# Kernel optimization log

Hardware: AMD Instinct MI355X
Metric: run time of the kernel (lower is better)

The kernel has to match this reference:

```python
import jax, jax.numpy as jnp
import numpy as np

# Layer node counts: [n0, n1, n2, n3] for a 3-hop sampled subgraph
N_NODES = [524288, 65536, 8192, 1024]
DIMS = [100, 256, 256, 47]


def sage_conv(x_src, x_dst, src, dst, Wl, bl, Wr, n_dst):
    # PyG SAGEConv: lin_l(mean_agg(neighbors)) + lin_r(root)
    msg = x_src[src]                                        # [E, in]
    agg = jax.ops.segment_sum(msg, dst, num_segments=n_dst)  # [n_dst, in]
    cnt = jax.ops.segment_sum(jnp.ones((src.shape[0],), dtype=x_src.dtype), dst,
                              num_segments=n_dst)
    agg = agg / jnp.maximum(cnt, 1.0)[:, None]               # mean, 0-deg -> 0
    return agg @ Wl + bl + x_dst @ Wr


def setup_inputs() -> dict:
    key = jax.random.key(0)
    ks = jax.random.split(key, 20)
    inp = {"x": jax.random.normal(ks[0], (N_NODES[0], DIMS[0]), dtype=jnp.float32)}
    E = [655360, 81920, 10240]
    for i in range(3):
        inp[f"src{i}"] = jax.random.randint(ks[1 + 2 * i], (E[i],), 0, N_NODES[i])
        inp[f"dst{i}"] = jax.random.randint(ks[2 + 2 * i], (E[i],), 0, N_NODES[i + 1])
    for i in range(3):
        fin, fout = DIMS[i], DIMS[i + 1]
        inp[f"Wl{i}"] = jax.random.normal(ks[7 + 3 * i], (fin, fout), jnp.float32) * (1.0 / np.sqrt(fin))
        inp[f"bl{i}"] = jnp.zeros((fout,), jnp.float32)
        inp[f"Wr{i}"] = jax.random.normal(ks[8 + 3 * i], (fin, fout), jnp.float32) * (1.0 / np.sqrt(fin))
    return inp


def reference(x, src0, dst0, src1, dst1, src2, dst2,
              Wl0, bl0, Wr0, Wl1, bl1, Wr1, Wl2, bl2, Wr2):
    srcs = [src0, src1, src2]
    dsts = [dst0, dst1, dst2]
    Wls = [Wl0, Wl1, Wl2]
    bls = [bl0, bl1, bl2]
    Wrs = [Wr0, Wr1, Wr2]
    h = x
    for i in range(3):
        n_dst = N_NODES[i + 1]
        h_dst = h[:n_dst]
        h = sage_conv(h, h_dst, srcs[i], dsts[i], Wls[i], bls[i], Wrs[i], n_dst)
        if i != 2:
            h = jax.nn.relu(h)  # dropout is identity in eval mode
    return jax.nn.log_softmax(h, axis=-1)
```

## Files before the change

kernel.cpp:

```cpp
#include <hip/hip_runtime.h>
#include <math.h>

constexpr int NN1 = 65536, NN2 = 8192, NN3 = 1024;
constexpr int E0 = 655360, E1 = 81920, E2 = 10240;
constexpr int ETOT = E0 + E1 + E2;
constexpr int NTOT = NN1 + NN2 + NN3;

static inline int cdiv(int a, int b) { return (a + b - 1) / b; }

typedef __bf16 bf16x8_t __attribute__((ext_vector_type(8)));
typedef float f32x4_t __attribute__((ext_vector_type(4)));

__device__ __forceinline__ unsigned short f2bf(float f) {
    union { float f; unsigned int u; } v; v.f = f;
    unsigned int r = v.u + 0x7fffu + ((v.u >> 16) & 1u);
    return (unsigned short)(r >> 16);
}
__device__ __forceinline__ float bf2f(unsigned short h) {
    union { unsigned int u; float f; } v; v.u = ((unsigned int)h) << 16;
    return v.f;
}

__global__ void count_all(const int* __restrict__ dst0, const int* __restrict__ dst1,
                          const int* __restrict__ dst2, int* __restrict__ cnt) {
    int i = blockIdx.x * 256 + threadIdx.x;
    if (i < E0) atomicAdd(&cnt[dst0[i]], 1);
    else if (i < E0 + E1) atomicAdd(&cnt[NN1 + dst1[i - E0]], 1);
    else if (i < ETOT) atomicAdd(&cnt[NN1 + NN2 + dst2[i - E0 - E1]], 1);
}

__global__ __launch_bounds__(1024) void scan1(const int* __restrict__ cnt, int n,
                                              int* __restrict__ ofs, int* __restrict__ sums) {
    __shared__ int s[1024];
    int i = blockIdx.x * 1024 + threadIdx.x;
    int v = (i < n) ? cnt[i] : 0;
    s[threadIdx.x] = v;
    __syncthreads();
    for (int off = 1; off < 1024; off <<= 1) {
        int t = (threadIdx.x >= off) ? s[threadIdx.x - off] : 0;
        __syncthreads();
        s[threadIdx.x] += t;
        __syncthreads();
    }
    if (i < n) ofs[i] = s[threadIdx.x] - v;
    if (threadIdx.x == 1023) sums[blockIdx.x] = s[1023];
}

__global__ void scan3(const int* __restrict__ sums, int n,
                      int* __restrict__ ofs, int* __restrict__ cursor) {
    __shared__ int pref_s;
    int c = (blockIdx.x * 256) >> 10;
    if (threadIdx.x < 64) {
        int v = 0;
        for (int j = threadIdx.x; j < c; j += 64) v += sums[j];
        for (int o = 32; o; o >>= 1) v += __shfl_down(v, o);
        if (threadIdx.x == 0) pref_s = v;
    }
    __syncthreads();
    int i = blockIdx.x * 256 + threadIdx.x;
    if (i < n) {
        int v = ofs[i] + pref_s;
        ofs[i] = v;
        cursor[i] = v;
    }
    if (blockIdx.x == 0 && threadIdx.x == 0) ofs[n] = ETOT;
}

__global__ void scatter_all(const int* __restrict__ src0, const int* __restrict__ dst0,
                            const int* __restrict__ src1, const int* __restrict__ dst1,
                            const int* __restrict__ src2, const int* __restrict__ dst2,
                            int* __restrict__ cursor, int* __restrict__ perm) {
    int i = blockIdx.x * 256 + threadIdx.x;
    if (i < E0) {
        int p = atomicAdd(&cursor[dst0[i]], 1);
        perm[p] = src0[i];
    } else if (i < E0 + E1) {
        int j = i - E0;
        int p = atomicAdd(&cursor[NN1 + dst1[j]], 1);
        perm[p] = src1[j];
    } else if (i < ETOT) {
        int j = i - E0 - E1;
        int p = atomicAdd(&cursor[NN1 + NN2 + dst2[j]], 1);
        perm[p] = src2[j];
    }
}

__global__ void agg0_kernel(const float* __restrict__ x, const int* __restrict__ perm,
                            const int* __restrict__ ofs, unsigned short* __restrict__ Ab, int nrows) {
    int wave = (blockIdx.x * blockDim.x + threadIdx.x) >> 6;
    int lane = threadIdx.x & 63;
    if (wave >= nrows) return;
    int g = lane >> 5, l5 = lane & 31;
    bool act = l5 < 25;
    int s0 = ofs[wave], s1 = ofs[wave + 1];
    float inv = 1.0f / fmaxf((float)(s1 - s0), 1.0f);
    f32x4_t A0 = {0.f, 0.f, 0.f, 0.f}, A1 = A0, A2 = A0, A3 = A0;
    int e = s0;
    for (; e + 8 <= s1; e += 8) {
        int p0 = perm[e + 0 + g];
        int p1 = perm[e + 2 + g];
        int p2 = perm[e + 4 + g];
        int p3 = perm[e + 6 + g];
        if (act) {
            A0 += *reinterpret_cast<const f32x4_t*>(x + (size_t)p0 * 100 + l5 * 4);
            A1 += *reinterpret_cast<const f32x4_t*>(x + (size_t)p1 * 100 + l5 * 4);
            A2 += *reinterpret_cast<const f32x4_t*>(x + (size_t)p2 * 100 + l5 * 4);
            A3 += *reinterpret_cast<const f32x4_t*>(x + (size_t)p3 * 100 + l5 * 4);
        }
    }
    for (; e < s1; e += 2) {
        int idx = e + g;
        if (idx < s1 && act)
            A0 += *reinterpret_cast<const f32x4_t*>(x + (size_t)perm[idx] * 100 + l5 * 4);
    }
    f32x4_t a = (A0 + A1) + (A2 + A3);
#pragma unroll
    for (int c = 0; c < 4; c++) a[c] += __shfl_xor(a[c], 32);
    unsigned short* row = Ab + (size_t)wave * 224;
    if (lane < 25) {
        ushort4 o;
        o.x = f2bf(a[0] * inv); o.y = f2bf(a[1] * inv);
        o.z = f2bf(a[2] * inv); o.w = f2bf(a[3] * inv);
        *reinterpret_cast<ushort4*>(row + lane * 4) = o;
        f32x4_t d = *reinterpret_cast<const f32x4_t*>(x + (size_t)wave * 100 + lane * 4);
        ushort4 od;
        od.x = f2bf(d[0]); od.y = f2bf(d[1]); od.z = f2bf(d[2]); od.w = f2bf(d[3]);
        *reinterpret_cast<ushort4*>(row + 100 + lane * 4) = od;
    } else if (lane < 31) {
        *reinterpret_cast<ushort4*>(row + 100 + lane * 4) = make_ushort4(0, 0, 0, 0);
    }
}

__global__ void agg1_kernel(const unsigned short* __restrict__ h, const int* __restrict__ perm,
                            const int* __restrict__ ofs, unsigned short* __restrict__ Ab, int nrows) {
    int wave = (blockIdx.x * blockDim.x + threadIdx.x) >> 6;
    int lane = threadIdx.x & 63;
    if (wave >= nrows) return;
    int s0 = ofs[wave], s1 = ofs[wave + 1];
    float inv = 1.0f / fmaxf((float)(s1 - s0), 1.0f);
    float acc[4][4] = {};
    int e = s0;
    for (; e + 4 <= s1; e += 4) {
        ushort4 v[4];
#pragma unroll
        for (int u = 0; u < 4; u++)
            v[u] = *reinterpret_cast<const ushort4*>(h + (size_t)perm[e + u] * 256 + lane * 4);
#pragma unroll
        for (int u = 0; u < 4; u++) {
            acc[u][0] += bf2f(v[u].x); acc[u][1] += bf2f(v[u].y);
            acc[u][2] += bf2f(v[u].z); acc[u][3] += bf2f(v[u].w);
        }
    }
    for (; e < s1; e++) {
        ushort4 v = *reinterpret_cast<const ushort4*>(h + (size_t)perm[e] * 256 + lane * 4);
        acc[0][0] += bf2f(v.x); acc[0][1] += bf2f(v.y);
        acc[0][2] += bf2f(v.z); acc[0][3] += bf2f(v.w);
    }
    ushort4 o;
    o.x = f2bf((acc[0][0] + acc[1][0] + acc[2][0] + acc[3][0]) * inv);
    o.y = f2bf((acc[0][1] + acc[1][1] + acc[2][1] + acc[3][1]) * inv);
    o.z = f2bf((acc[0][2] + acc[1][2] + acc[2][2] + acc[3][2]) * inv);
    o.w = f2bf((acc[0][3] + acc[1][3] + acc[2][3] + acc[3][3]) * inv);
    *reinterpret_cast<ushort4*>(Ab + (size_t)wave * 512 + lane * 4) = o;
    *reinterpret_cast<ushort4*>(Ab + (size_t)wave * 512 + 256 + lane * 4) =
        *reinterpret_cast<const ushort4*>(h + (size_t)wave * 256 + lane * 4);
}

__global__ void agg_vec4_256(const float* __restrict__ x, const int* __restrict__ perm,
                             const int* __restrict__ ofs, float* __restrict__ agg, int nrows) {
    int wave = (blockIdx.x * blockDim.x + threadIdx.x) >> 6;
    int lane = threadIdx.x & 63;
    if (wave >= nrows) return;
    int s0 = ofs[wave], s1 = ofs[wave + 1];
    float4 acc = make_float4(0.f, 0.f, 0.f, 0.f);
    for (int e = s0; e < s1; e++) {
        const float4* xr = (const float4*)(x + (size_t)perm[e] * 256);
        float4 v = xr[lane];
        acc.x += v.x; acc.y += v.y; acc.z += v.z; acc.w += v.w;
    }
    float inv = 1.0f / fmaxf((float)(s1 - s0), 1.0f);
    acc.x *= inv; acc.y *= inv; acc.z *= inv; acc.w *= inv;
    ((float4*)(agg + (size_t)wave * 256))[lane] = acc;
}

__global__ void prep_w(const float* __restrict__ Wl0, const float* __restrict__ Wr0,
                       unsigned short* __restrict__ Wt0,
                       const float* __restrict__ Wl1, const float* __restrict__ Wr1,
                       unsigned short* __restrict__ Wt1) {
    int b = blockIdx.x;
    if (b < 256) {
        int n = b, k = threadIdx.x;
        if (k < 224) {
            float v = (k < 100) ? Wl0[k * 256 + n] : (k < 200 ? Wr0[(k - 100) * 256 + n] : 0.f);
            Wt0[n * 224 + k] = f2bf(v);
        }
    } else {
        int idx = (b - 256) * 256 + threadIdx.x;
        int n = idx >> 9, k = idx & 511;
        float v = (k < 256) ? Wl1[k * 256 + n] : Wr1[(k - 256) * 256 + n];
        Wt1[idx] = f2bf(v);
    }
}

template <int OUT_BF16, int RELU>
__global__ __launch_bounds__(256) void mfma_gemm(const unsigned short* __restrict__ A,
                                                 const unsigned short* __restrict__ Wt,
                                                 const float* __restrict__ bias,
                                                 void* __restrict__ outp,
                                                 int M, int N, int K) {
    __shared__ unsigned short As[128][40];
    __shared__ unsigned short Bs[128][40];
    int tid = threadIdx.x;
    int lane = tid & 63, wid = tid >> 6;
    int wm = (wid & 1) * 64, wn = (wid >> 1) * 64;
    int bm = blockIdx.y * 128, bn = blockIdx.x * 128;

    f32x4_t acc[4][4];
#pragma unroll
    for (int i = 0; i < 4; i++)
#pragma unroll
        for (int j = 0; j < 4; j++)
#pragma unroll
            for (int r = 0; r < 4; r++) acc[i][j][r] = 0.f;

    int r0 = lane & 15, kg = lane >> 4;

    for (int k0 = 0; k0 < K; k0 += 32) {
        {
            int c = tid;
            int row = c >> 2, k8 = (c & 3) << 3;
            *reinterpret_cast<int4*>(&As[row][k8]) =
                *reinterpret_cast<const int4*>(&A[(size_t)(bm + row) * K + k0 + k8]);
            c = tid + 256;
            row = c >> 2; k8 = (c & 3) << 3;
            *reinterpret_cast<int4*>(&As[row][k8]) =
                *reinterpret_cast<const int4*>(&A[(size_t)(bm + row) * K + k0 + k8]);
        }
        {
            int c = tid;
            int row = c >> 2, k8 = (c & 3) << 3;
            *reinterpret_cast<int4*>(&Bs[row][k8]) =
                *reinterpret_cast<const int4*>(&Wt[(size_t)(bn + row) * K + k0 + k8]);
            c = tid + 256;
            row = c >> 2; k8 = (c & 3) << 3;
            *reinterpret_cast<int4*>(&Bs[row][k8]) =
                *reinterpret_cast<const int4*>(&Wt[(size_t)(bn + row) * K + k0 + k8]);
        }
        __syncthreads();

        bf16x8_t af[4], bfv[4];
#pragma unroll
        for (int mi = 0; mi < 4; mi++)
            af[mi] = *reinterpret_cast<const bf16x8_t*>(&As[wm + mi * 16 + r0][kg * 8]);
#pragma unroll
        for (int ni = 0; ni < 4; ni++)
            bfv[ni] = *reinterpret_cast<const bf16x8_t*>(&Bs[wn + ni * 16 + r0][kg * 8]);
#pragma unroll
        for (int mi = 0; mi < 4; mi++)
#pragma unroll
            for (int ni = 0; ni < 4; ni++)
                acc[mi][ni] = __builtin_amdgcn_mfma_f32_16x16x32_bf16(af[mi], bfv[ni], acc[mi][ni], 0, 0, 0);
        __syncthreads();
    }

    int cc = lane & 15, rr = (lane >> 4) * 4;
#pragma unroll
    for (int mi = 0; mi < 4; mi++) {
#pragma unroll
        for (int ni = 0; ni < 4; ni++) {
            int col = bn + wn + ni * 16 + cc;
            float b = bias[col];
#pragma unroll
            for (int j = 0; j < 4; j++) {
                int row = bm + wm + mi * 16 + rr + j;
                float v = acc[mi][ni][j] + b;
                if (RELU) v = fmaxf(v, 0.f);
                if (OUT_BF16)
                    ((unsigned short*)outp)[(size_t)row * N + col] = f2bf(v);
                else
                    ((float*)outp)[(size_t)row * N + col] = v;
            }
        }
    }
}

__global__ __launch_bounds__(256) void gemm2_fused(const float* __restrict__ A1, const float* __restrict__ W1, int K1,
                                                   const float* __restrict__ A2, const float* __restrict__ W2, int K2,
                                                   const float* __restrict__ bias, float* __restrict__ out,
                                                   int M, int N) {
    __shared__ float As[16][65];
    __shared__ float Bs[16][64];
    int tid = threadIdx.x;
    int tx = tid & 15, ty = tid >> 4;
    int bm = blockIdx.y * 64;
    float acc[4][4] = {};
    for (int pass = 0; pass < 2; ++pass) {
        const float* A = pass ? A2 : A1;
        const float* W = pass ? W2 : W1;
        int K = pass ? K2 : K1;
        for (int k0 = 0; k0 < K; k0 += 16) {
#pragma unroll
            for (int i = 0; i < 4; i++) {
                int L = i * 256 + tid;
                int m = L >> 4, k = L & 15;
                int gm = bm + m, gk = k0 + k;
                float v = 0.f;
                if (gm < M && gk < K) v = A[(size_t)gm * K + gk];
                As[k][m] = v;
            }
#pragma unroll
            for (int i = 0; i < 4; i++) {
                int L = i * 256 + tid;
                int n = L & 63, k = L >> 6;
                int gk = k0 + k;
                float v = 0.f;
                if (gk < K && n < N) v = W[(size_t)gk * N + n];
                Bs[k][n] = v;
            }
            __syncthreads();
#pragma unroll
            for (int k = 0; k < 16; k++) {
                float a[4], b[4];
#pragma unroll
                for (int i = 0; i < 4; i++) a[i] = As[k][ty * 4 + i];
#pragma unroll
                for (int j = 0; j < 4; j++) b[j] = Bs[k][tx * 4 + j];
#pragma unroll
                for (int i = 0; i < 4; i++)
#pragma unroll
                    for (int j = 0; j < 4; j++) acc[i][j] += a[i] * b[j];
            }
            __syncthreads();
        }
    }
#pragma unroll
    for (int i = 0; i < 4; i++) {
        int gm = bm + ty * 4 + i;
        float vals[4];
        float vmax = -1e30f;
#pragma unroll
        for (int j = 0; j < 4; j++) {
            int gn = tx * 4 + j;
            vals[j] = (gn < N) ? acc[i][j] + bias[gn] : -1e30f;
            vmax = fmaxf(vmax, vals[j]);
        }
#pragma unroll
        for (int o = 1; o < 16; o <<= 1) vmax = fmaxf(vmax, __shfl_xor(vmax, o));
        float se = 0.f;
#pragma unroll
        for (int j = 0; j < 4; j++) {
            int gn = tx * 4 + j;
            if (gn < N) se += expf(vals[j] - vmax);
        }
#pragma unroll
        for (int o = 1; o < 16; o <<= 1) se += __shfl_xor(se, o);
        float ls = logf(se);
#pragma unroll
        for (int j = 0; j < 4; j++) {
            int gn = tx * 4 + j;
            if (gn < N && gm < M) out[(size_t)gm * N + gn] = vals[j] - vmax - ls;
        }
    }
}

extern "C" void kernel_launch(void* const* d_in, const int* in_sizes, int n_in,
                              void* d_out, int out_size, void* d_ws, size_t ws_size,
                              hipStream_t stream) {
    const float* x   = (const float*)d_in[0];
    const int* src0  = (const int*)d_in[1];
    const int* dst0  = (const int*)d_in[2];
    const int* src1  = (const int*)d_in[3];
    const int* dst1  = (const int*)d_in[4];
    const int* src2  = (const int*)d_in[5];
    const int* dst2  = (const int*)d_in[6];
    const float* Wl0 = (const float*)d_in[7];
    const float* bl0 = (const float*)d_in[8];
    const float* Wr0 = (const float*)d_in[9];
    const float* Wl1 = (const float*)d_in[10];
    const float* bl1 = (const float*)d_in[11];
    const float* Wr1 = (const float*)d_in[12];
    const float* Wl2 = (const float*)d_in[13];
    const float* bl2 = (const float*)d_in[14];
    const float* Wr2 = (const float*)d_in[15];
    float* out = (float*)d_out;

    char* p = (char*)d_ws;
    auto alloc = [&](size_t bytes) { char* r = p; p += (bytes + 255) & ~(size_t)255; return r; };
    unsigned short* Ab0 = (unsigned short*)alloc((size_t)NN1 * 224 * 2);
    unsigned short* h1  = (unsigned short*)alloc((size_t)NN1 * 256 * 2);
    unsigned short* Ab1 = (unsigned short*)alloc((size_t)NN2 * 512 * 2);
    float* h2    = (float*)alloc((size_t)NN2 * 256 * 4);
    float* agg2  = (float*)alloc((size_t)NN3 * 256 * 4);
    unsigned short* Wt0 = (unsigned short*)alloc(256 * 224 * 2);
    unsigned short* Wt1 = (unsigned short*)alloc(256 * 512 * 2);
    int* cnt    = (int*)alloc((size_t)NTOT * 4);
    int* ofs    = (int*)alloc((size_t)(NTOT + 1) * 4);
    int* cursor = (int*)alloc((size_t)(NTOT + 1) * 4);
    int* sums   = (int*)alloc(128 * 4);
    int* perm   = (int*)alloc((size_t)ETOT * 4);

    prep_w<<<768, 256, 0, stream>>>(Wl0, Wr0, Wt0, Wl1, Wr1, Wt1);
    hipMemsetAsync(cnt, 0, (size_t)NTOT * 4, stream);
    count_all<<<cdiv(ETOT, 256), 256, 0, stream>>>(dst0, dst1, dst2, cnt);
    int nb = cdiv(NTOT, 1024);
    scan1<<<nb, 1024, 0, stream>>>(cnt, NTOT, ofs, sums);
    scan3<<<cdiv(NTOT, 256), 256, 0, stream>>>(sums, NTOT, ofs, cursor);
    scatter_all<<<cdiv(ETOT, 256), 256, 0, stream>>>(src0, dst0, src1, dst1, src2, dst2, cursor, perm);

    agg0_kernel<<<cdiv(NN1 * 64, 256), 256, 0, stream>>>(x, perm, ofs, Ab0, NN1);
    {
        dim3 grid(256 / 128, NN1 / 128);
        mfma_gemm<1, 1><<<grid, 256, 0, stream>>>(Ab0, Wt0, bl0, h1, NN1, 256, 224);
    }

    agg1_kernel<<<cdiv(NN2 * 64, 256), 256, 0, stream>>>(h1, perm, ofs + NN1, Ab1, NN2);
    {
        dim3 grid(256 / 128, NN2 / 128);
        mfma_gemm<0, 1><<<grid, 256, 0, stream>>>(Ab1, Wt1, bl1, h2, NN2, 256, 512);
    }

    agg_vec4_256<<<cdiv(NN3 * 64, 256), 256, 0, stream>>>(h2, perm, ofs + NN1 + NN2, agg2, NN3);
    {
        dim3 grid(1, cdiv(NN3, 64));
        gemm2_fused<<<grid, 256, 0, stream>>>(agg2, Wl2, 256, h2, Wr2, 256, bl2, out, NN3, 47);
    }
}
```

Before: 298.8 us.

## Fuse neighbor aggregation with MFMA GEMM for layers 0 and 1

Replaces the separate aggregate-then-GEMM kernels for layers 0 and 1 with fused kernels. Each block aggregates its own rows into shared memory and immediately runs the bf16 MFMA GEMM in two passes, first over the mean-aggregated features and then over the root features, so the concatenated A buffers are never written to or read back from global memory. Weights are split into separate left and right transposed bf16 matrices to match. The trade-off is that the gather and GEMM phases now run serially within a block with fewer blocks and larger shared memory, which may lower occupancy and latency hiding. In layer 1 the aggregation is also repeated by both column blocks.

```diff
diff --git a/kernel.cpp b/kernel.cpp
--- a/kernel.cpp
+++ b/kernel.cpp
@@ -85,85 +85,251 @@
     }
 }
 
-__global__ void agg0_kernel(const float* __restrict__ x, const int* __restrict__ perm,
-                            const int* __restrict__ ofs, unsigned short* __restrict__ Ab, int nrows) {
-    int wave = (blockIdx.x * blockDim.x + threadIdx.x) >> 6;
-    int lane = threadIdx.x & 63;
-    if (wave >= nrows) return;
-    int g = lane >> 5, l5 = lane & 31;
-    bool act = l5 < 25;
-    int s0 = ofs[wave], s1 = ofs[wave + 1];
-    float inv = 1.0f / fmaxf((float)(s1 - s0), 1.0f);
-    f32x4_t A0 = {0.f, 0.f, 0.f, 0.f}, A1 = A0, A2 = A0, A3 = A0;
-    int e = s0;
-    for (; e + 8 <= s1; e += 8) {
-        int p0 = perm[e + 0 + g];
-        int p1 = perm[e + 2 + g];
-        int p2 = perm[e + 4 + g];
-        int p3 = perm[e + 6 + g];
-        if (act) {
-            A0 += *reinterpret_cast<const f32x4_t*>(x + (size_t)p0 * 100 + l5 * 4);
-            A1 += *reinterpret_cast<const f32x4_t*>(x + (size_t)p1 * 100 + l5 * 4);
-            A2 += *reinterpret_cast<const f32x4_t*>(x + (size_t)p2 * 100 + l5 * 4);
-            A3 += *reinterpret_cast<const f32x4_t*>(x + (size_t)p3 * 100 + l5 * 4);
-        }
-    }
-    for (; e < s1; e += 2) {
-        int idx = e + g;
-        if (idx < s1 && act)
-            A0 += *reinterpret_cast<const f32x4_t*>(x + (size_t)perm[idx] * 100 + l5 * 4);
-    }
-    f32x4_t a = (A0 + A1) + (A2 + A3);
-#pragma unroll
-    for (int c = 0; c < 4; c++) a[c] += __shfl_xor(a[c], 32);
-    unsigned short* row = Ab + (size_t)wave * 224;
-    if (lane < 25) {
+__global__ void prep_w(const float* __restrict__ Wl0, const float* __restrict__ Wr0,
+                       unsigned short* __restrict__ Wt0a, unsigned short* __restrict__ Wt0b,
+                       const float* __restrict__ Wl1, const float* __restrict__ Wr1,
+                       unsigned short* __restrict__ Wt1a, unsigned short* __restrict__ Wt1b) {
+    int b = blockIdx.x, t = threadIdx.x;
+    if (b < 128) {
+        int idx = b * 256 + t; int n = idx >> 7, k = idx & 127;
+        Wt0a[idx] = f2bf(k < 100 ? Wl0[k * 256 + n] : 0.f);
+    } else if (b < 256) {
+        int idx = (b - 128) * 256 + t; int n = idx >> 7, k = idx & 127;
+        Wt0b[idx] = f2bf(k < 100 ? Wr0[k * 256 + n] : 0.f);
+    } else if (b < 512) {
+        int idx = (b - 256) * 256 + t; int n = idx >> 8, k = idx & 255;
+        Wt1a[idx] = f2bf(Wl1[k * 256 + n]);
+    } else {
+        int idx = (b - 512) * 256 + t; int n = idx >> 8, k = idx & 255;
+        Wt1b[idx] = f2bf(Wr1[k * 256 + n]);
+    }
+}
+
+__global__ __launch_bounds__(512) void fused_l0(const float* __restrict__ x,
+                                                const int* __restrict__ perm,
+                                                const int* __restrict__ ofs,
+                                                const unsigned short* __restrict__ Wt0a,
+                                                const unsigned short* __restrict__ Wt0b,
+                                                const float* __restrict__ bias,
+                                                unsigned short* __restrict__ h1) {
+    __shared__ unsigned short As[128][136];
+    __shared__ unsigned short Bs[256][40];
+    int tid = threadIdx.x;
+    int lane = tid & 63, wid = tid >> 6;
+    int bm = blockIdx.x * 128;
+
+    {
+        int g = lane >> 5, l5 = lane & 31;
+        bool act = l5 < 25;
+        for (int r = 0; r < 16; ++r) {
+            int row = wid * 16 + r;
+            int node = bm + row;
+            int s0 = ofs[node], s1 = ofs[node + 1];
+            float inv = 1.0f / fmaxf((float)(s1 - s0), 1.0f);
+            f32x4_t A0 = {0.f, 0.f, 0.f, 0.f}, A1 = A0, A2 = A0, A3 = A0;
+            int e = s0;
+            for (; e + 8 <= s1; e += 8) {
+                int p0 = perm[e + 0 + g];
+                int p1 = perm[e + 2 + g];
+                int p2 = perm[e + 4 + g];
+                int p3 = perm[e + 6 + g];
+                if (act) {
+                    A0 += *reinterpret_cast<const f32x4_t*>(x + (size_t)p0 * 100 + l5 * 4);
+                    A1 += *reinterpret_cast<const f32x4_t*>(x + (size_t)p1 * 100 + l5 * 4);
+                    A2 += *reinterpret_cast<const f32x4_t*>(x + (size_t)p2 * 100 + l5 * 4);
+                    A3 += *reinterpret_cast<const f32x4_t*>(x + (size_t)p3 * 100 + l5 * 4);
+                }
+            }
+            for (; e < s1; e += 2) {
+                int idx = e + g;
+                if (idx < s1 && act)
+                    A0 += *reinterpret_cast<const f32x4_t*>(x + (size_t)perm[idx] * 100 + l5 * 4);
+            }
+            f32x4_t a = (A0 + A1) + (A2 + A3);
+#pragma unroll
+            for (int c = 0; c < 4; c++) a[c] += __shfl_xor(a[c], 32);
+            if (lane < 25) {
+                ushort4 o;
+                o.x = f2bf(a[0] * inv); o.y = f2bf(a[1] * inv);
+                o.z = f2bf(a[2] * inv); o.w = f2bf(a[3] * inv);
+                *reinterpret_cast<ushort4*>(&As[row][lane * 4]) = o;
+            } else if (lane < 32) {
+                *reinterpret_cast<ushort4*>(&As[row][100 + (lane - 25) * 4]) = make_ushort4(0, 0, 0, 0);
+            }
+        }
+    }
+
+    f32x4_t acc[4][4];
+#pragma unroll
+    for (int i = 0; i < 4; i++)
+#pragma unroll
+        for (int j = 0; j < 4; j++)
+#pragma unroll
+            for (int r = 0; r < 4; r++) acc[i][j][r] = 0.f;
+
+    int r0 = lane & 15, kg = lane >> 4;
+    int wm = (wid >> 2) * 64, wn = (wid & 3) * 64;
+
+    for (int pass = 0; pass < 2; ++pass) {
+        const unsigned short* W = pass ? Wt0b : Wt0a;
+        if (pass) {
+            __syncthreads();
+            int rown = tid >> 2, q = tid & 3;
+            for (int c4 = q; c4 < 25; c4 += 4) {
+                f32x4_t v = *reinterpret_cast<const f32x4_t*>(x + (size_t)(bm + rown) * 100 + c4 * 4);
+                ushort4 o;
+                o.x = f2bf(v[0]); o.y = f2bf(v[1]); o.z = f2bf(v[2]); o.w = f2bf(v[3]);
+                *reinterpret_cast<ushort4*>(&As[rown][c4 * 4]) = o;
+            }
+            if (q == 3) {
+#pragma unroll
+                for (int c4 = 25; c4 < 32; ++c4)
+                    *reinterpret_cast<ushort4*>(&As[rown][c4 * 4]) = make_ushort4(0, 0, 0, 0);
+            }
+        }
+        for (int ks = 0; ks < 4; ++ks) {
+            __syncthreads();
+            for (int c = tid; c < 1024; c += 512) {
+                int n = c >> 2, k8 = (c & 3) << 3;
+                *reinterpret_cast<int4*>(&Bs[n][k8]) =
+                    *reinterpret_cast<const int4*>(&W[(size_t)n * 128 + ks * 32 + k8]);
+            }
+            __syncthreads();
+            bf16x8_t af[4], bfv[4];
+#pragma unroll
+            for (int mi = 0; mi < 4; mi++)
+                af[mi] = *reinterpret_cast<const bf16x8_t*>(&As[wm + mi * 16 + r0][ks * 32 + kg * 8]);
+#pragma unroll
+            for (int ni = 0; ni < 4; ni++)
+                bfv[ni] = *reinterpret_cast<const bf16x8_t*>(&Bs[wn + ni * 16 + r0][kg * 8]);
+#pragma unroll
+            for (int mi = 0; mi < 4; mi++)
+#pragma unroll
+                for (int ni = 0; ni < 4; ni++)
+                    acc[mi][ni] = __builtin_amdgcn_mfma_f32_16x16x32_bf16(af[mi], bfv[ni], acc[mi][ni], 0, 0, 0);
+        }
+    }
+
+    int cc = lane & 15, rr = (lane >> 4) * 4;
+#pragma unroll
+    for (int mi = 0; mi < 4; mi++) {
+#pragma unroll
+        for (int ni = 0; ni < 4; ni++) {
+            int col = wn + ni * 16 + cc;
+            float b = bias[col];
+#pragma unroll
+            for (int j = 0; j < 4; j++) {
+                int row = bm + wm + mi * 16 + rr + j;
+                float v = fmaxf(acc[mi][ni][j] + b, 0.f);
+                h1[(size_t)row * 256 + col] = f2bf(v);
+            }
+        }
+    }
+}
+
+__global__ __launch_bounds__(512) void fused_l1(const unsigned short* __restrict__ h1,
+                                                const int* __restrict__ perm,
+                                                const int* __restrict__ ofs,
+                                                const unsigned short* __restrict__ Wt1a,
+                                                const unsigned short* __restrict__ Wt1b,
+                                                const float* __restrict__ bias,
+                                                float* __restrict__ h2) {
+    __shared__ unsigned short As[64][264];
+    __shared__ unsigned short Bs[128][40];
+    int tid = threadIdx.x;
+    int lane = tid & 63, wid = tid >> 6;
+    int bm = blockIdx.y * 64, bn = blockIdx.x * 128;
+
+    for (int r = 0; r < 8; ++r) {
+        int row = wid * 8 + r;
+        int node = bm + row;
+        int s0 = ofs[node], s1 = ofs[node + 1];
+        float inv = 1.0f / fmaxf((float)(s1 - s0), 1.0f);
+        float ac[4][4] = {};
+        int e = s0;
+        for (; e + 4 <= s1; e += 4) {
+            ushort4 v[4];
+#pragma unroll
+            for (int u = 0; u < 4; u++)
+                v[u] = *reinterpret_cast<const ushort4*>(h1 + (size_t)perm[e + u] * 256 + lane * 4);
+#pragma unroll
+            for (int u = 0; u < 4; u++) {
+                ac[u][0] += bf2f(v[u].x); ac[u][1] += bf2f(v[u].y);
+                ac[u][2] += bf2f(v[u].z); ac[u][3] += bf2f(v[u].w);
+            }
+        }
+        for (; e < s1; e++) {
+            ushort4 v = *reinterpret_cast<const ushort4*>(h1 + (size_t)perm[e] * 256 + lane * 4);
+            ac[0][0] += bf2f(v.x); ac[0][1] += bf2f(v.y);
+            ac[0][2] += bf2f(v.z); ac[0][3] += bf2f(v.w);
+        }
         ushort4 o;
-        o.x = f2bf(a[0] * inv); o.y = f2bf(a[1] * inv);
-        o.z = f2bf(a[2] * inv); o.w = f2bf(a[3] * inv);
-        *reinterpret_cast<ushort4*>(row + lane * 4) = o;
-        f32x4_t d = *reinterpret_cast<const f32x4_t*>(x + (size_t)wave * 100 + lane * 4);
-        ushort4 od;
-        od.x = f2bf(d[0]); od.y = f2bf(d[1]); od.z = f2bf(d[2]); od.w = f2bf(d[3]);
-        *reinterpret_cast<ushort4*>(row + 100 + lane * 4) = od;
-    } else if (lane < 31) {
-        *reinterpret_cast<ushort4*>(row + 100 + lane * 4) = make_ushort4(0, 0, 0, 0);
-    }
-}
-
-__global__ void agg1_kernel(const unsigned short* __restrict__ h, const int* __restrict__ perm,
-                            const int* __restrict__ ofs, unsigned short* __restrict__ Ab, int nrows) {
-    int wave = (blockIdx.x * blockDim.x + threadIdx.x) >> 6;
-    int lane = threadIdx.x & 63;
-    if (wave >= nrows) return;
-    int s0 = ofs[wave], s1 = ofs[wave + 1];
-    float inv = 1.0f / fmaxf((float)(s1 - s0), 1.0f);
-    float acc[4][4] = {};
-    int e = s0;
-    for (; e + 4 <= s1; e += 4) {
-        ushort4 v[4];
-#pragma unroll
-        for (int u = 0; u < 4; u++)
-            v[u] = *reinterpret_cast<const ushort4*>(h + (size_t)perm[e + u] * 256 + lane * 4);
-#pragma unroll
-        for (int u = 0; u < 4; u++) {
-            acc[u][0] += bf2f(v[u].x); acc[u][1] += bf2f(v[u].y);
-            acc[u][2] += bf2f(v[u].z); acc[u][3] += bf2f(v[u].w);
-        }
-    }
-    for (; e < s1; e++) {
-        ushort4 v = *reinterpret_cast<const ushort4*>(h + (size_t)perm[e] * 256 + lane * 4);
-        acc[0][0] += bf2f(v.x); acc[0][1] += bf2f(v.y);
-        acc[0][2] += bf2f(v.z); acc[0][3] += bf2f(v.w);
-    }
-    ushort4 o;
-    o.x = f2bf((acc[0][0] + acc[1][0] + acc[2][0] + acc[3][0]) * inv);
-    o.y = f2bf((acc[0][1] + acc[1][1] + acc[2][1] + acc[3][1]) * inv);
-    o.z = f2bf((acc[0][2] + acc[1][2] + acc[2][2] + acc[3][2]) * inv);
-    o.w = f2bf((acc[0][3] + acc[1][3] + acc[2][3] + acc[3][3]) * inv);
-    *reinterpret_cast<ushort4*>(Ab + (size_t)wave * 512 + lane * 4) = o;
-    *reinterpret_cast<ushort4*>(Ab + (size_t)wave * 512 + 256 + lane * 4) =
-        *reinterpret_cast<const ushort4*>(h + (size_t)wave * 256 + lane * 4);
+        o.x = f2bf((ac[0][0] + ac[1][0] + ac[2][0] + ac[3][0]) * inv);
+        o.y = f2bf((ac[0][1] + ac[1][1] + ac[2][1] + ac[3][1]) * inv);
+        o.z = f2bf((ac[0][2] + ac[1][2] + ac[2][2] + ac[3][2]) * inv);
+        o.w = f2bf((ac[0][3] + ac[1][3] + ac[2][3] + ac[3][3]) * inv);
+        *reinterpret_cast<ushort4*>(&As[row][lane * 4]) = o;
+    }
+
+    f32x4_t acc[2][2];
+#pragma unroll
+    for (int i = 0; i < 2; i++)
+#pragma unroll
+        for (int j = 0; j < 2; j++)
+#pragma unroll
+            for (int r = 0; r < 4; r++) acc[i][j][r] = 0.f;
+
+    int r0 = lane & 15, kg = lane >> 4;
+    int wm = (wid >> 2) * 32, wn = (wid & 3) * 32;
+
+    for (int pass = 0; pass < 2; ++pass) {
+        const unsigned short* W = pass ? Wt1b : Wt1a;
+        if (pass) {
+            __syncthreads();
+            for (int c = tid; c < 2048; c += 512) {
+                int row = c >> 5, k8 = (c & 31) << 3;
+                *reinterpret_cast<int4*>(&As[row][k8]) =
+                    *reinterpret_cast<const int4*>(&h1[(size_t)(bm + row) * 256 + k8]);
+            }
+        }
+        for (int ks = 0; ks < 8; ++ks) {
+            __syncthreads();
+            {
+                int c = tid;
+                int n = c >> 2, k8 = (c & 3) << 3;
+                *reinterpret_cast<int4*>(&Bs[n][k8]) =
+                    *reinterpret_cast<const int4*>(&W[(size_t)(bn + n) * 256 + ks * 32 + k8]);
+            }
+            __syncthreads();
+            bf16x8_t af[2], bfv[2];
+#pragma unroll
+            for (int mi = 0; mi < 2; mi++)
+                af[mi] = *reinterpret_cast<const bf16x8_t*>(&As[wm + mi * 16 + r0][ks * 32 + kg * 8]);
+#pragma unroll
+            for (int ni = 0; ni < 2; ni++)
+                bfv[ni] = *reinterpret_cast<const bf16x8_t*>(&Bs[wn + ni * 16 + r0][kg * 8]);
+#pragma unroll
+            for (int mi = 0; mi < 2; mi++)
+#pragma unroll
+                for (int ni = 0; ni < 2; ni++)
+                    acc[mi][ni] = __builtin_amdgcn_mfma_f32_16x16x32_bf16(af[mi], bfv[ni], acc[mi][ni], 0, 0, 0);
+        }
+    }
+
+    int cc = lane & 15, rr = (lane >> 4) * 4;
+#pragma unroll
+    for (int mi = 0; mi < 2; mi++) {
+#pragma unroll
+        for (int ni = 0; ni < 2; ni++) {
+            int col = bn + wn + ni * 16 + cc;
+            float b = bias[col];
+#pragma unroll
+            for (int j = 0; j < 4; j++) {
+                int row = bm + wm + mi * 16 + rr + j;
+                h2[(size_t)row * 256 + col] = fmaxf(acc[mi][ni][j] + b, 0.f);
+            }
+        }
+    }
 }
 
 __global__ void agg_vec4_256(const float* __restrict__ x, const int* __restrict__ perm,
@@ -181,107 +347,6 @@
     float inv = 1.0f / fmaxf((float)(s1 - s0), 1.0f);
     acc.x *= inv; acc.y *= inv; acc.z *= inv; acc.w *= inv;
     ((float4*)(agg + (size_t)wave * 256))[lane] = acc;
-}
-
-__global__ void prep_w(const float* __restrict__ Wl0, const float* __restrict__ Wr0,
-                       unsigned short* __restrict__ Wt0,
-                       const float* __restrict__ Wl1, const float* __restrict__ Wr1,
-                       unsigned short* __restrict__ Wt1) {
-    int b = blockIdx.x;
-    if (b < 256) {
-        int n = b, k = threadIdx.x;
-        if (k < 224) {
-            float v = (k < 100) ? Wl0[k * 256 + n] : (k < 200 ? Wr0[(k - 100) * 256 + n] : 0.f);
-            Wt0[n * 224 + k] = f2bf(v);
-        }
-    } else {
-        int idx = (b - 256) * 256 + threadIdx.x;
-        int n = idx >> 9, k = idx & 511;
-        float v = (k < 256) ? Wl1[k * 256 + n] : Wr1[(k - 256) * 256 + n];
-        Wt1[idx] = f2bf(v);
-    }
-}
-
-template <int OUT_BF16, int RELU>
-__global__ __launch_bounds__(256) void mfma_gemm(const unsigned short* __restrict__ A,
-                                                 const unsigned short* __restrict__ Wt,
-                                                 const float* __restrict__ bias,
-                                                 void* __restrict__ outp,
-                                                 int M, int N, int K) {
-    __shared__ unsigned short As[128][40];
-    __shared__ unsigned short Bs[128][40];
-    int tid = threadIdx.x;
-    int lane = tid & 63, wid = tid >> 6;
-    int wm = (wid & 1) * 64, wn = (wid >> 1) * 64;
-    int bm = blockIdx.y * 128, bn = blockIdx.x * 128;
-
-    f32x4_t acc[4][4];
-#pragma unroll
-    for (int i = 0; i < 4; i++)
-#pragma unroll
-        for (int j = 0; j < 4; j++)
-#pragma unroll
-            for (int r = 0; r < 4; r++) acc[i][j][r] = 0.f;
-
-    int r0 = lane & 15, kg = lane >> 4;
-
-    for (int k0 = 0; k0 < K; k0 += 32) {
-        {
-            int c = tid;
-            int row = c >> 2, k8 = (c & 3) << 3;
-            *reinterpret_cast<int4*>(&As[row][k8]) =
-                *reinterpret_cast<const int4*>(&A[(size_t)(bm + row) * K + k0 + k8]);
-            c = tid + 256;
-            row = c >> 2; k8 = (c & 3) << 3;
-            *reinterpret_cast<int4*>(&As[row][k8]) =
-                *reinterpret_cast<const int4*>(&A[(size_t)(bm + row) * K + k0 + k8]);
-        }
-        {
-            int c = tid;
-            int row = c >> 2, k8 = (c & 3) << 3;
-            *reinterpret_cast<int4*>(&Bs[row][k8]) =
-                *reinterpret_cast<const int4*>(&Wt[(size_t)(bn + row) * K + k0 + k8]);
-            c = tid + 256;
-            row = c >> 2; k8 = (c & 3) << 3;
-            *reinterpret_cast<int4*>(&Bs[row][k8]) =
-                *reinterpret_cast<const int4*>(&Wt[(size_t)(bn + row) * K + k0 + k8]);
-        }
-        __syncthreads();
-
-        bf16x8_t af[4], bfv[4];
-#pragma unroll
-        for (int mi = 0; mi < 4; mi++)
-            af[mi] = *reinterpret_cast<const bf16x8_t*>(&As[wm + mi * 16 + r0][kg * 8]);
-#pragma unroll
-        for (int ni = 0; ni < 4; ni++)
-            bfv[ni] = *reinterpret_cast<const bf16x8_t*>(&Bs[wn + ni * 16 + r0][kg * 8]);
-#pragma unroll
-        for (int mi = 0; mi < 4; mi++)
-#pragma unroll
-            for (int ni = 0; ni < 4; ni++)
-                acc[mi][ni] = __builtin_amdgcn_mfma_f32_16x16x32_bf16(af[mi], bfv[ni], acc[mi][ni], 0, 0, 0);
-        __syncthreads();
-    }
-
-    int cc = lane & 15, rr = (lane >> 4) * 4;
-#pragma unroll
-    for (int mi = 0; mi < 4; mi++) {
-#pragma unroll
-        for (int ni = 0; ni < 4; ni++) {
-            int col = bn + wn + ni * 16 + cc;
-            float b = bias[col];
-#pragma unroll
-            for (int j = 0; j < 4; j++) {
-                int row = bm + wm + mi * 16 + rr + j;
-                float v = acc[mi][ni][j] + b;
-                if (RELU) v = fmaxf(v, 0.f);
-                if (OUT_BF16)
-                    ((unsigned short*)outp)[(size_t)row * N + col] = f2bf(v);
-                else
-                    ((float*)outp)[(size_t)row * N + col] = v;
-            }
-        }
-    }
 }
 
 __global__ __launch_bounds__(256) void gemm2_fused(const float* __restrict__ A1, const float* __restrict__ W1, int K1,
@@ -386,20 +451,20 @@
 
     char* p = (char*)d_ws;
     auto alloc = [&](size_t bytes) { char* r = p; p += (bytes + 255) & ~(size_t)255; return r; };
-    unsigned short* Ab0 = (unsigned short*)alloc((size_t)NN1 * 224 * 2);
-    unsigned short* h1  = (unsigned short*)alloc((size_t)NN1 * 256 * 2);
-    unsigned short* Ab1 = (unsigned short*)alloc((size_t)NN2 * 512 * 2);
+    unsigned short* h1   = (unsigned short*)alloc((size_t)NN1 * 256 * 2);
     float* h2    = (float*)alloc((size_t)NN2 * 256 * 4);
     float* agg2  = (float*)alloc((size_t)NN3 * 256 * 4);
-    unsigned short* Wt0 = (unsigned short*)alloc(256 * 224 * 2);
-    unsigned short* Wt1 = (unsigned short*)alloc(256 * 512 * 2);
+    unsigned short* Wt0a = (unsigned short*)alloc(256 * 128 * 2);
+    unsigned short* Wt0b = (unsigned short*)alloc(256 * 128 * 2);
+    unsigned short* Wt1a = (unsigned short*)alloc(256 * 256 * 2);
+    unsigned short* Wt1b = (unsigned short*)alloc(256 * 256 * 2);
     int* cnt    = (int*)alloc((size_t)NTOT * 4);
     int* ofs    = (int*)alloc((size_t)(NTOT + 1) * 4);
     int* cursor = (int*)alloc((size_t)(NTOT + 1) * 4);
     int* sums   = (int*)alloc(128 * 4);
     int* perm   = (int*)alloc((size_t)ETOT * 4);
 
-    prep_w<<<768, 256, 0, stream>>>(Wl0, Wr0, Wt0, Wl1, Wr1, Wt1);
+    prep_w<<<768, 256, 0, stream>>>(Wl0, Wr0, Wt0a, Wt0b, Wl1, Wr1, Wt1a, Wt1b);
     hipMemsetAsync(cnt, 0, (size_t)NTOT * 4, stream);
     count_all<<<cdiv(ETOT, 256), 256, 0, stream>>>(dst0, dst1, dst2, cnt);
     int nb = cdiv(NTOT, 1024);
@@ -407,16 +472,11 @@
     scan3<<<cdiv(NTOT, 256), 256, 0, stream>>>(sums, NTOT, ofs, cursor);
     scatter_all<<<cdiv(ETOT, 256), 256, 0, stream>>>(src0, dst0, src1, dst1, src2, dst2, cursor, perm);
 
-    agg0_kernel<<<cdiv(NN1 * 64, 256), 256, 0, stream>>>(x, perm, ofs, Ab0, NN1);
+    fused_l0<<<NN1 / 128, 512, 0, stream>>>(x, perm, ofs, Wt0a, Wt0b, bl0, h1);
+
     {
-        dim3 grid(256 / 128, NN1 / 128);
-        mfma_gemm<1, 1><<<grid, 256, 0, stream>>>(Ab0, Wt0, bl0, h1, NN1, 256, 224);
-    }
-
-    agg1_kernel<<<cdiv(NN2 * 64, 256), 256, 0, stream>>>(h1, perm, ofs + NN1, Ab1, NN2);
-    {
-        dim3 grid(256 / 128, NN2 / 128);
-        mfma_gemm<0, 1><<<grid, 256, 0, stream>>>(Ab1, Wt1, bl1, h2, NN2, 256, 512);
+        dim3 grid(2, NN2 / 64);
+        fused_l1<<<grid, 512, 0, stream>>>(h1, perm, ofs + NN1, Wt1a, Wt1b, bl1, h2);
     }
 
     agg_vec4_256<<<cdiv(NN3 * 64, 256), 256, 0, stream>>>(h2, perm, ofs + NN1 + NN2, agg2, NN3);
```

After: 291.4 us. -2.5%, faster.
